# Optimization experiments

Measured on AMD Instinct MI355X. Metric: run time of the kernel, lower is better.

Reference implementation:

```python
import jax, jax.numpy as jnp
import numpy as np

EPS = 1e-6

def elu_feature_map(x):
    # phi(x) = elu(x) + 1 (always positive)
    return jax.nn.elu(x) + 1.0

def setup_inputs() -> dict:
    key = jax.random.key(0)
    kq, kk, kv = jax.random.split(key, 3)
    B, T, H, E = 2, 4096, 8, 64
    return {
        "query": jax.random.normal(kq, (B, T, H, E), dtype=jnp.float32),
        "key": jax.random.normal(kk, (B, T, H, E), dtype=jnp.float32),
        "value": jax.random.normal(kv, (B, T, H, E), dtype=jnp.float32),
    }

def reference(query, key, value):
    # b t h e -> b h t e
    q = jnp.transpose(query, (0, 2, 1, 3))
    k = jnp.transpose(key, (0, 2, 1, 3))
    v = jnp.transpose(value, (0, 2, 1, 3))
    Q = elu_feature_map(q)  # [b,h,t,e]
    K = elu_feature_map(k)  # [b,h,t,e]
    # Causal linear attention: running sums over the sequence axis.
    # KV_cum[t] = sum_{s<=t} K_s (outer) V_s  -> [b,h,t,e,d]
    kv = jnp.einsum('bhte,bhtd->bhted', K, v)
    kv_cum = jnp.cumsum(kv, axis=2)
    k_cum = jnp.cumsum(K, axis=2)  # [b,h,t,e]
    # Normalizer Z_t = 1 / (Q_t . sum_{s<=t} K_s + eps)
    Z = 1.0 / (jnp.einsum('bhte,bhte->bht', Q, k_cum) + EPS)
    out = jnp.einsum('bhte,bhted->bhtd', Q, kv_cum) * Z[..., None]
    # b h t d -> b t h d
    return jnp.transpose(out, (0, 2, 1, 3))
```

## Files before the change

### kernel.cpp

```cpp
#include <hip/hip_runtime.h>
#include <math.h>

#define B 2
#define T 4096
#define H 8
#define E 64
#define D 64
#define C 128
#define NC (T / C)
#define BH (B * H)
#define EPS 1e-6f
#define PT 132
#define PQ 72
#define PBT 200
typedef short short8 __attribute__((ext_vector_type(8)));
typedef short short4v __attribute__((ext_vector_type(4)));
typedef float f32x4 __attribute__((ext_vector_type(4)));

__device__ __forceinline__ float phi(float x) {
    return x > 0.0f ? x + 1.0f : __expf(x);
}
__device__ __forceinline__ ushort f2bf(float f) {
    uint u = __float_as_uint(f);
    return (ushort)((u + 0x7FFFu + ((u >> 16) & 1u)) >> 16);
}
__device__ __forceinline__ float bf2f(ushort h) {
    return __uint_as_float(((uint)h) << 16);
}

__global__ __launch_bounds__(256) void k_chunk_sums(
        const float* __restrict__ Kg, const float* __restrict__ Vg,
        float* __restrict__ SpartT, float* __restrict__ zpart,
        ushort* __restrict__ VTg) {
    int blk = blockIdx.x;
    int bh = blk / NC, c = blk % NC;
    int b = bh / H, h = bh % H;
    int t0 = c * C;
    __shared__ ushort sKt[E][PT];
    __shared__ ushort sVt[D][PT];
    int tid = threadIdx.x;
    int lane = tid & 63, w = tid >> 6;
    const float4* Kg4 = (const float4*)Kg;
    const float4* Vg4 = (const float4*)Vg;

    for (int l = tid; l < C * E / 4; l += 256) {
        int i = l >> 4, e4 = l & 15;
        size_t g = ((size_t)(b * T + t0 + i) * H + h) * 16 + e4;
        float4 kv = Kg4[g];
        float pk[4] = {phi(kv.x), phi(kv.y), phi(kv.z), phi(kv.w)};
        float4 vv = Vg4[g];
        float pv[4] = {vv.x, vv.y, vv.z, vv.w};
        #pragma unroll
        for (int cc = 0; cc < 4; ++cc) {
            sKt[e4 * 4 + cc][i] = f2bf(pk[cc]);
            sVt[e4 * 4 + cc][i] = f2bf(pv[cc]);
        }
    }
    __syncthreads();

    float* Sp = SpartT + (size_t)blk * (E * D);
    #pragma unroll
    for (int tt = 0; tt < 4; ++tt) {
        int idx = w * 4 + tt;
        int mt = idx >> 2, nt = idx & 3;
        int am = mt * 16 + (lane & 15);
        int bn = nt * 16 + (lane & 15);
        int kb = (lane >> 4) * 8;
        f32x4 acc = {};
        #pragma unroll
        for (int ks = 0; ks < 4; ++ks) {
            short8 a  = *(const short8*)&sVt[am][ks * 32 + kb];
            short8 bb = *(const short8*)&sKt[bn][ks * 32 + kb];
            acc = __builtin_amdgcn_mfma_f32_16x16x32_bf16(a, bb, acc, 0, 0, 0);
        }
        #pragma unroll
        for (int r = 0; r < 4; ++r) {
            int drow = mt * 16 + (lane >> 4) * 4 + r;
            Sp[drow * E + bn] = acc[r];
        }
    }
    ushort* vt = VTg + (size_t)blk * (C * D);
    for (int l = tid; l < C * D / 8; l += 256) {
        int d = l >> 4, p = l & 15;
        *(short8*)&vt[d * C + p * 8] = *(const short8*)&sVt[d][p * 8];
    }
    if (tid < E) {
        float s = 0.0f;
        #pragma unroll
        for (int p = 0; p < 16; ++p) {
            short8 v = *(const short8*)&sKt[tid][p * 8];
            #pragma unroll
            for (int j = 0; j < 8; ++j) s += bf2f((ushort)v[j]);
        }
        zpart[(size_t)blk * E + tid] = s;
    }
}

__global__ __launch_bounds__(256) void k_scan(
        float* __restrict__ SpartT, float* __restrict__ zpart) {
    int bh  = blockIdx.x / 17;
    int sub = blockIdx.x % 17;
    int tid = threadIdx.x;
    if (sub < 16) {
        int l = sub * 256 + tid;
        float* base = SpartT + (size_t)bh * NC * (E * D) + l;
        float vals[NC];
        #pragma unroll
        for (int c = 0; c < NC; ++c) vals[c] = base[(size_t)c * (E * D)];
        float run = 0.0f;
        #pragma unroll
        for (int c = 0; c < NC; ++c) {
            base[(size_t)c * (E * D)] = run;
            run += vals[c];
        }
    } else if (tid < E) {
        float* base = zpart + (size_t)bh * NC * E + tid;
        float vals[NC];
        #pragma unroll
        for (int c = 0; c < NC; ++c) vals[c] = base[(size_t)c * E];
        float run = 0.0f;
        #pragma unroll
        for (int c = 0; c < NC; ++c) {
            base[(size_t)c * E] = run;
            run += vals[c];
        }
    }
}

__global__ __launch_bounds__(512, 4) void k_output(
        const float* __restrict__ Qg, const float* __restrict__ Kg,
        const ushort* __restrict__ VTg, const float* __restrict__ SpartT,
        const float* __restrict__ zpart, float* __restrict__ Og) {
    int blk = blockIdx.x;
    int bh = blk / NC, c = blk % NC;
    int b = bh / H, h = bh % H;
    int t0 = c * C;

    __shared__ ushort sQ[C][PQ];
    __shared__ ushort sKB[64 * PBT];
    __shared__ ushort sA[C][C];
    __shared__ float  sDen[C];
    __shared__ float  sZ[E];

    int tid = threadIdx.x;
    int lane = tid & 63;
    int w = tid >> 6;

    const float4* Qg4 = (const float4*)Qg;
    const float4* Kg4 = (const float4*)Kg;

    for (int l = tid; l < C * 8; l += 512) {
        int i = l >> 3, e8 = l & 7;
        size_t g = ((size_t)(b * T + t0 + i) * H + h) * 16 + e8 * 2;
        float4 qa = Qg4[g], qb = Qg4[g + 1];
        short8 qv;
        qv[0] = (short)f2bf(phi(qa.x)); qv[1] = (short)f2bf(phi(qa.y));
        qv[2] = (short)f2bf(phi(qa.z)); qv[3] = (short)f2bf(phi(qa.w));
        qv[4] = (short)f2bf(phi(qb.x)); qv[5] = (short)f2bf(phi(qb.y));
        qv[6] = (short)f2bf(phi(qb.z)); qv[7] = (short)f2bf(phi(qb.w));
        *(short8*)&sQ[i][e8 * 8] = qv;
        float4 ka = Kg4[g], kb = Kg4[g + 1];
        short8 kv;
        kv[0] = (short)f2bf(phi(ka.x)); kv[1] = (short)f2bf(phi(ka.y));
        kv[2] = (short)f2bf(phi(ka.z)); kv[3] = (short)f2bf(phi(ka.w));
        kv[4] = (short)f2bf(phi(kb.x)); kv[5] = (short)f2bf(phi(kb.y));
        kv[6] = (short)f2bf(phi(kb.z)); kv[7] = (short)f2bf(phi(kb.w));
        *(short8*)&sKB[i * PQ + e8 * 8] = kv;
    }
    {
        short8 zz = {0, 0, 0, 0, 0, 0, 0, 0};
        ushort* af = (ushort*)sA;
        #pragma unroll
        for (int it = 0; it < 4; ++it)
            *(short8*)&af[(tid + 512 * it) * 8] = zz;
    }
    const short8* vt8 = (const short8*)(VTg + (size_t)blk * (C * D));
    short8 vtreg[2];
    #pragma unroll
    for (int it = 0; it < 2; ++it) vtreg[it] = vt8[tid * 2 + it];
    const float4* Sp4 = (const float4*)(SpartT + (size_t)blk * (E * D));
    float4 s0reg[2];
    #pragma unroll
    for (int it = 0; it < 2; ++it) s0reg[it] = Sp4[tid * 2 + it];
    if (tid < E) sZ[tid] = zpart[(size_t)blk * E + tid];
    __syncthreads();

    for (int idx = w; idx < 36; idx += 8) {
        int tr = 0;
        while ((tr + 1) * (tr + 2) / 2 <= idx) ++tr;
        int tc = idx - tr * (tr + 1) / 2;
        int am = tr * 16 + (lane & 15);
        int bn = tc * 16 + (lane & 15);
        int kb = (lane >> 4) * 8;
        f32x4 acc = {};
        #pragma unroll
        for (int ks = 0; ks < 2; ++ks) {
            short8 a  = *(const short8*)&sQ[am][ks * 32 + kb];
            short8 bb = *(const short8*)&sKB[bn * PQ + ks * 32 + kb];
            acc = __builtin_amdgcn_mfma_f32_16x16x32_bf16(a, bb, acc, 0, 0, 0);
        }
        int colb = tc * 16 + (lane & 15);
        #pragma unroll
        for (int r = 0; r < 4; ++r) {
            int row = tr * 16 + (lane >> 4) * 4 + r;
            if (tr == tc && colb > row) continue;
            sA[row][colb ^ ((row & 7) << 3)] = f2bf(acc[r]);
        }
    }
    __syncthreads();

    #pragma unroll
    for (int it = 0; it < 2; ++it) {
        int idx = tid * 2 + it;
        int d = idx >> 4, p = idx & 15;
        *(short8*)&sKB[d * PBT + p * 8] = vtreg[it];
    }
    #pragma unroll
    for (int it = 0; it < 2; ++it) {
        int idx = tid * 2 + it;
        int d = idx >> 4, e0 = (idx & 15) * 4;
        float4 s = s0reg[it];
        short4v sv;
        sv[0] = (short)f2bf(s.x); sv[1] = (short)f2bf(s.y);
        sv[2] = (short)f2bf(s.z); sv[3] = (short)f2bf(s.w);
        *(short4v*)&sKB[d * PBT + 128 + e0] = sv;
    }
    if (tid < 256) {
        int row = tid >> 1, hf = tid & 1;
        float s = 0.0f;
        const ushort* ar = &sA[row][hf * 64];
        #pragma unroll
        for (int q8 = 0; q8 < 8; ++q8) {
            int cq = (q8 + row) & 7;
            short8 v = *(const short8*)&ar[cq * 8];
            #pragma unroll
            for (int j = 0; j < 8; ++j) s += bf2f((ushort)v[j]);
        }
        const ushort* qr = &sQ[row][0];
        #pragma unroll
        for (int e = 0; e < 32; ++e) {
            int ee = hf * 32 + e;
            s += bf2f(qr[ee]) * sZ[ee];
        }
        s += __shfl_xor(s, 1);
        if (hf == 0) sDen[row] = s;
    }
    __syncthreads();

    {
        int tcn = w & 3;
        int trb = w >> 2;
        int ncol = tcn * 16 + (lane & 15);
        int g8 = (lane >> 4) * 8;
        #pragma unroll
        for (int rt = 0; rt < 4; ++rt) {
            int tr = trb + rt * 2;
            int m0 = tr * 16;
            int arow = m0 + (lane & 15);
            int aswz = arow & 7;
            f32x4 acc = {};
            int smax = (m0 + 15) >> 5;
            for (int s = 0; s <= smax; ++s) {
                int chunk = s * 4 + (lane >> 4);
                short8 a  = *(const short8*)&sA[arow][(chunk ^ aswz) * 8];
                short8 bb = *(const short8*)&sKB[ncol * PBT + s * 32 + g8];
                acc = __builtin_amdgcn_mfma_f32_16x16x32_bf16(a, bb, acc, 0, 0, 0);
            }
            #pragma unroll
            for (int s = 0; s < 2; ++s) {
                short8 a  = *(const short8*)&sQ[arow][s * 32 + g8];
                short8 bb = *(const short8*)&sKB[ncol * PBT + 128 + s * 32 + g8];
                acc = __builtin_amdgcn_mfma_f32_16x16x32_bf16(a, bb, acc, 0, 0, 0);
            }
            #pragma unroll
            for (int r = 0; r < 4; ++r) {
                int row = m0 + (lane >> 4) * 4 + r;
                float z = 1.0f / (sDen[row] + EPS);
                Og[((size_t)(b * T + t0 + row) * H + h) * 64 + ncol] = acc[r] * z;
            }
        }
    }
}

extern "C" void kernel_launch(void* const* d_in, const int* in_sizes, int n_in,
                              void* d_out, int out_size, void* d_ws, size_t ws_size,
                              hipStream_t stream) {
    const float* q = (const float*)d_in[0];
    const float* k = (const float*)d_in[1];
    const float* v = (const float*)d_in[2];
    float* out = (float*)d_out;

    float*  SpartT = (float*)d_ws;
    float*  zpart  = SpartT + (size_t)BH * NC * E * D;
    ushort* VTg    = (ushort*)(zpart + (size_t)BH * NC * E);

    k_chunk_sums<<<BH * NC, 256, 0, stream>>>(k, v, SpartT, zpart, VTg);
    k_scan<<<BH * 17, 256, 0, stream>>>(SpartT, zpart);
    k_output<<<BH * NC, 512, 0, stream>>>(q, k, VTg, SpartT, zpart, out);
}
```

Baseline: 35.22 us.

## Fold normalizer into MFMA, cache phi(K) in bf16, restructure output tiling

```diff
diff --git a/kernel.cpp b/kernel.cpp
--- a/kernel.cpp
+++ b/kernel.cpp
@@ -1,4 +1,5 @@
 #include <hip/hip_runtime.h>
+#include <hip/hip_bf16.h>
 #include <math.h>
 
 #define B 2
@@ -13,25 +14,26 @@
 #define PT 132
 #define PQ 72
 #define PBT 200
+
 typedef short short8 __attribute__((ext_vector_type(8)));
-typedef short short4v __attribute__((ext_vector_type(4)));
 typedef float f32x4 __attribute__((ext_vector_type(4)));
 
 __device__ __forceinline__ float phi(float x) {
     return x > 0.0f ? x + 1.0f : __expf(x);
+}
+__device__ __forceinline__ uint pk2(float a, float b) {
+    __hip_bfloat162 h = __float22bfloat162_rn(make_float2(a, b));
+    union { __hip_bfloat162 h2; uint u; } cv; cv.h2 = h; return cv.u;
 }
 __device__ __forceinline__ ushort f2bf(float f) {
     uint u = __float_as_uint(f);
     return (ushort)((u + 0x7FFFu + ((u >> 16) & 1u)) >> 16);
 }
-__device__ __forceinline__ float bf2f(ushort h) {
-    return __uint_as_float(((uint)h) << 16);
-}
 
 __global__ __launch_bounds__(256) void k_chunk_sums(
         const float* __restrict__ Kg, const float* __restrict__ Vg,
         float* __restrict__ SpartT, float* __restrict__ zpart,
-        ushort* __restrict__ VTg) {
+        ushort* __restrict__ VTg, ushort* __restrict__ PKg) {
     int blk = blockIdx.x;
     int bh = blk / NC, c = blk % NC;
     int b = bh / H, h = bh % H;
@@ -42,75 +44,81 @@
     int lane = tid & 63, w = tid >> 6;
     const float4* Kg4 = (const float4*)Kg;
     const float4* Vg4 = (const float4*)Vg;
-
-    for (int l = tid; l < C * E / 4; l += 256) {
-        int i = l >> 4, e4 = l & 15;
-        size_t g = ((size_t)(b * T + t0 + i) * H + h) * 16 + e4;
-        float4 kv = Kg4[g];
-        float pk[4] = {phi(kv.x), phi(kv.y), phi(kv.z), phi(kv.w)};
-        float4 vv = Vg4[g];
-        float pv[4] = {vv.x, vv.y, vv.z, vv.w};
+    uint2* PK2 = (uint2*)(PKg + (size_t)blk * (C * E));
+
+    for (int l = tid; l < (C / 2) * 16; l += 256) {
+        int i2 = l >> 4, e4 = l & 15;
+        int t = i2 * 2;
+        size_t g0 = ((size_t)(b * T + t0 + t) * H + h) * 16 + e4;
+        size_t g1 = g0 + H * 16;
+        float4 ka = Kg4[g0], kb = Kg4[g1];
+        float4 va = Vg4[g0], vb = Vg4[g1];
+        float pk0[4] = {phi(ka.x), phi(ka.y), phi(ka.z), phi(ka.w)};
+        float pk1[4] = {phi(kb.x), phi(kb.y), phi(kb.z), phi(kb.w)};
+        float pv0[4] = {va.x, va.y, va.z, va.w};
+        float pv1[4] = {vb.x, vb.y, vb.z, vb.w};
         #pragma unroll
         for (int cc = 0; cc < 4; ++cc) {
-            sKt[e4 * 4 + cc][i] = f2bf(pk[cc]);
-            sVt[e4 * 4 + cc][i] = f2bf(pv[cc]);
-        }
-    }
-    __syncthreads();
-
-    float* Sp = SpartT + (size_t)blk * (E * D);
-    #pragma unroll
-    for (int tt = 0; tt < 4; ++tt) {
-        int idx = w * 4 + tt;
-        int mt = idx >> 2, nt = idx & 3;
-        int am = mt * 16 + (lane & 15);
-        int bn = nt * 16 + (lane & 15);
-        int kb = (lane >> 4) * 8;
-        f32x4 acc = {};
-        #pragma unroll
+            *(uint*)&sKt[e4 * 4 + cc][t] = pk2(pk0[cc], pk1[cc]);
+            *(uint*)&sVt[e4 * 4 + cc][t] = pk2(pv0[cc], pv1[cc]);
+        }
+        PK2[t * 16 + e4]       = make_uint2(pk2(pk0[0], pk0[1]), pk2(pk0[2], pk0[3]));
+        PK2[(t + 1) * 16 + e4] = make_uint2(pk2(pk1[0], pk1[1]), pk2(pk1[2], pk1[3]));
+    }
+    __syncthreads();
+
+    {
+        int g = lane >> 4, cl = lane & 15;
+        int mt = w;
+        f32x4 acc[4] = {};
         for (int ks = 0; ks < 4; ++ks) {
-            short8 a  = *(const short8*)&sVt[am][ks * 32 + kb];
-            short8 bb = *(const short8*)&sKt[bn][ks * 32 + kb];
-            acc = __builtin_amdgcn_mfma_f32_16x16x32_bf16(a, bb, acc, 0, 0, 0);
-        }
-        #pragma unroll
-        for (int r = 0; r < 4; ++r) {
-            int drow = mt * 16 + (lane >> 4) * 4 + r;
-            Sp[drow * E + bn] = acc[r];
+            short8 a = *(const short8*)&sKt[mt * 16 + cl][ks * 32 + g * 8];
+            #pragma unroll
+            for (int nt = 0; nt < 4; ++nt) {
+                short8 bb = *(const short8*)&sVt[nt * 16 + cl][ks * 32 + g * 8];
+                acc[nt] = __builtin_amdgcn_mfma_f32_16x16x32_bf16(a, bb, acc[nt], 0, 0, 0);
+            }
+        }
+        float* Sp = SpartT + (size_t)blk * (E * D);
+        #pragma unroll
+        for (int nt = 0; nt < 4; ++nt) {
+            int d = nt * 16 + cl;
+            *(float4*)&Sp[d * E + mt * 16 + g * 4] =
+                make_float4(acc[nt][0], acc[nt][1], acc[nt][2], acc[nt][3]);
         }
     }
     ushort* vt = VTg + (size_t)blk * (C * D);
-    for (int l = tid; l < C * D / 8; l += 256) {
-        int d = l >> 4, p = l & 15;
-        *(short8*)&vt[d * C + p * 8] = *(const short8*)&sVt[d][p * 8];
-    }
+    for (int l = tid; l < C * D / 8; l += 256)
+        *(short8*)&vt[(l >> 4) * C + (l & 15) * 8] = *(const short8*)&sVt[l >> 4][(l & 15) * 8];
     if (tid < E) {
         float s = 0.0f;
         #pragma unroll
         for (int p = 0; p < 16; ++p) {
             short8 v = *(const short8*)&sKt[tid][p * 8];
             #pragma unroll
-            for (int j = 0; j < 8; ++j) s += bf2f((ushort)v[j]);
+            for (int j = 0; j < 8; ++j) s += __uint_as_float(((uint)(ushort)v[j]) << 16);
         }
         zpart[(size_t)blk * E + tid] = s;
     }
 }
 
 __global__ __launch_bounds__(256) void k_scan(
-        float* __restrict__ SpartT, float* __restrict__ zpart) {
+        const float* __restrict__ SpartT, float* __restrict__ zpart,
+        ushort* __restrict__ S0bf) {
     int bh  = blockIdx.x / 17;
     int sub = blockIdx.x % 17;
     int tid = threadIdx.x;
     if (sub < 16) {
         int l = sub * 256 + tid;
-        float* base = SpartT + (size_t)bh * NC * (E * D) + l;
+        const float* base = SpartT + (size_t)bh * NC * (E * D) + l;
+        ushort* obase = S0bf + (size_t)bh * NC * (E * D) + l;
         float vals[NC];
         #pragma unroll
         for (int c = 0; c < NC; ++c) vals[c] = base[(size_t)c * (E * D)];
         float run = 0.0f;
         #pragma unroll
         for (int c = 0; c < NC; ++c) {
-            base[(size_t)c * (E * D)] = run;
+            obase[(size_t)c * (E * D)] = f2bf(run);
             run += vals[c];
         }
     } else if (tid < E) {
@@ -128,8 +136,8 @@
 }
 
 __global__ __launch_bounds__(512, 4) void k_output(
-        const float* __restrict__ Qg, const float* __restrict__ Kg,
-        const ushort* __restrict__ VTg, const float* __restrict__ SpartT,
+        const float* __restrict__ Qg, const ushort* __restrict__ PKg,
+        const ushort* __restrict__ VTg, const ushort* __restrict__ S0bf,
         const float* __restrict__ zpart, float* __restrict__ Og) {
     int blk = blockIdx.x;
     int bh = blk / NC, c = blk % NC;
@@ -137,147 +145,109 @@
     int t0 = c * C;
 
     __shared__ ushort sQ[C][PQ];
-    __shared__ ushort sKB[64 * PBT];
+    __shared__ ushort sKB[13000];
     __shared__ ushort sA[C][C];
-    __shared__ float  sDen[C];
-    __shared__ float  sZ[E];
 
     int tid = threadIdx.x;
     int lane = tid & 63;
     int w = tid >> 6;
+    int g = lane >> 4, cl = lane & 15;
 
     const float4* Qg4 = (const float4*)Qg;
-    const float4* Kg4 = (const float4*)Kg;
 
     for (int l = tid; l < C * 8; l += 512) {
         int i = l >> 3, e8 = l & 7;
-        size_t g = ((size_t)(b * T + t0 + i) * H + h) * 16 + e8 * 2;
-        float4 qa = Qg4[g], qb = Qg4[g + 1];
-        short8 qv;
-        qv[0] = (short)f2bf(phi(qa.x)); qv[1] = (short)f2bf(phi(qa.y));
-        qv[2] = (short)f2bf(phi(qa.z)); qv[3] = (short)f2bf(phi(qa.w));
-        qv[4] = (short)f2bf(phi(qb.x)); qv[5] = (short)f2bf(phi(qb.y));
-        qv[6] = (short)f2bf(phi(qb.z)); qv[7] = (short)f2bf(phi(qb.w));
-        *(short8*)&sQ[i][e8 * 8] = qv;
-        float4 ka = Kg4[g], kb = Kg4[g + 1];
-        short8 kv;
-        kv[0] = (short)f2bf(phi(ka.x)); kv[1] = (short)f2bf(phi(ka.y));
-        kv[2] = (short)f2bf(phi(ka.z)); kv[3] = (short)f2bf(phi(ka.w));
-        kv[4] = (short)f2bf(phi(kb.x)); kv[5] = (short)f2bf(phi(kb.y));
-        kv[6] = (short)f2bf(phi(kb.z)); kv[7] = (short)f2bf(phi(kb.w));
-        *(short8*)&sKB[i * PQ + e8 * 8] = kv;
-    }
-    {
-        short8 zz = {0, 0, 0, 0, 0, 0, 0, 0};
+        size_t gg = ((size_t)(b * T + t0 + i) * H + h) * 16 + e8 * 2;
+        float4 qa = Qg4[gg], qb = Qg4[gg + 1];
+        uint4 qv = make_uint4(pk2(phi(qa.x), phi(qa.y)), pk2(phi(qa.z), phi(qa.w)),
+                              pk2(phi(qb.x), phi(qb.y)), pk2(phi(qb.z), phi(qb.w)));
+        *(uint4*)&sQ[i][e8 * 8] = qv;
+    }
+    const short8* pk8 = (const short8*)(PKg + (size_t)blk * (C * E));
+    for (int l = tid; l < C * 8; l += 512)
+        *(short8*)&sKB[(l >> 3) * PQ + (l & 7) * 8] = pk8[l];
+    {
+        uint4 zz = make_uint4(0, 0, 0, 0);
         ushort* af = (ushort*)sA;
         #pragma unroll
         for (int it = 0; it < 4; ++it)
-            *(short8*)&af[(tid + 512 * it) * 8] = zz;
+            *(uint4*)&af[(tid + 512 * it) * 8] = zz;
     }
     const short8* vt8 = (const short8*)(VTg + (size_t)blk * (C * D));
-    short8 vtreg[2];
-    #pragma unroll
-    for (int it = 0; it < 2; ++it) vtreg[it] = vt8[tid * 2 + it];
-    const float4* Sp4 = (const float4*)(SpartT + (size_t)blk * (E * D));
-    float4 s0reg[2];
-    #pragma unroll
-    for (int it = 0; it < 2; ++it) s0reg[it] = Sp4[tid * 2 + it];
-    if (tid < E) sZ[tid] = zpart[(size_t)blk * E + tid];
+    short8 vt0 = vt8[tid * 2], vt1 = vt8[tid * 2 + 1];
+    short8 s0reg = ((const short8*)(S0bf + (size_t)blk * (E * D)))[tid];
+    float zreg = (tid < E) ? zpart[(size_t)blk * E + tid] : 0.0f;
     __syncthreads();
 
     for (int idx = w; idx < 36; idx += 8) {
         int tr = 0;
         while ((tr + 1) * (tr + 2) / 2 <= idx) ++tr;
         int tc = idx - tr * (tr + 1) / 2;
-        int am = tr * 16 + (lane & 15);
-        int bn = tc * 16 + (lane & 15);
-        int kb = (lane >> 4) * 8;
         f32x4 acc = {};
         #pragma unroll
         for (int ks = 0; ks < 2; ++ks) {
-            short8 a  = *(const short8*)&sQ[am][ks * 32 + kb];
-            short8 bb = *(const short8*)&sKB[bn * PQ + ks * 32 + kb];
-            acc = __builtin_amdgcn_mfma_f32_16x16x32_bf16(a, bb, acc, 0, 0, 0);
-        }
-        int colb = tc * 16 + (lane & 15);
+            short8 a  = *(const short8*)&sKB[(tc * 16 + cl) * PQ + ks * 32 + g * 8];
+            short8 bq = *(const short8*)&sQ[tr * 16 + cl][ks * 32 + g * 8];
+            acc = __builtin_amdgcn_mfma_f32_16x16x32_bf16(a, bq, acc, 0, 0, 0);
+        }
+        int iq = tr * 16 + cl;
+        int j0 = tc * 16 + g * 4;
+        float v0 = (j0 + 0 <= iq) ? acc[0] : 0.0f;
+        float v1 = (j0 + 1 <= iq) ? acc[1] : 0.0f;
+        float v2 = (j0 + 2 <= iq) ? acc[2] : 0.0f;
+        float v3 = (j0 + 3 <= iq) ? acc[3] : 0.0f;
+        int pb = (tc * 2 + (g >> 1)) ^ (iq & 7);
+        *(uint2*)&sA[iq][pb * 8 + (g & 1) * 4] = make_uint2(pk2(v0, v1), pk2(v2, v3));
+    }
+    __syncthreads();
+
+    {
+        int i0 = tid * 2, i1 = tid * 2 + 1;
+        *(short8*)&sKB[(i0 >> 4) * PBT + (i0 & 15) * 8] = vt0;
+        *(short8*)&sKB[(i1 >> 4) * PBT + (i1 & 15) * 8] = vt1;
+        *(short8*)&sKB[(tid >> 3) * PBT + 128 + (tid & 7) * 8] = s0reg;
+        if (tid < E) sKB[64 * PBT + 128 + tid] = f2bf(zreg);
+        else if (tid < E + 16) {
+            short8 ones = {16256, 16256, 16256, 16256, 16256, 16256, 16256, 16256};
+            *(short8*)&sKB[64 * PBT + (tid - E) * 8] = ones;
+        }
+    }
+    __syncthreads();
+
+    {
+        const int permv[8] = {0, 1, 2, 3, 6, 7, 4, 5};
+        int mt = permv[w];
+        int m0 = mt * 16;
+        int arow = m0 + cl;
+        int aswz = arow & 7;
+        int smax = (m0 + 15) >> 5;
+        f32x4 acc[5] = {};
+        for (int s = 0; s <= smax; ++s) {
+            short8 a = *(const short8*)&sA[arow][(((s * 4 + g) ^ aswz)) * 8];
+            #pragma unroll
+            for (int nt = 0; nt < 5; ++nt) {
+                short8 bb = *(const short8*)&sKB[(nt * 16 + cl) * PBT + s * 32 + g * 8];
+                acc[nt] = __builtin_amdgcn_mfma_f32_16x16x32_bf16(a, bb, acc[nt], 0, 0, 0);
+            }
+        }
+        #pragma unroll
+        for (int s2 = 0; s2 < 2; ++s2) {
+            short8 a = *(const short8*)&sQ[arow][s2 * 32 + g * 8];
+            #pragma unroll
+            for (int nt = 0; nt < 5; ++nt) {
+                short8 bb = *(const short8*)&sKB[(nt * 16 + cl) * PBT + 128 + s2 * 32 + g * 8];
+                acc[nt] = __builtin_amdgcn_mfma_f32_16x16x32_bf16(a, bb, acc[nt], 0, 0, 0);
+            }
+        }
         #pragma unroll
         for (int r = 0; r < 4; ++r) {
-            int row = tr * 16 + (lane >> 4) * 4 + r;
-            if (tr == tc && colb > row) continue;
-            sA[row][colb ^ ((row & 7) << 3)] = f2bf(acc[r]);
-        }
-    }
-    __syncthreads();
-
-    #pragma unroll
-    for (int it = 0; it < 2; ++it) {
-        int idx = tid * 2 + it;
-        int d = idx >> 4, p = idx & 15;
-        *(short8*)&sKB[d * PBT + p * 8] = vtreg[it];
-    }
-    #pragma unroll
-    for (int it = 0; it < 2; ++it) {
-        int idx = tid * 2 + it;
-        int d = idx >> 4, e0 = (idx & 15) * 4;
-        float4 s = s0reg[it];
-        short4v sv;
-        sv[0] = (short)f2bf(s.x); sv[1] = (short)f2bf(s.y);
-        sv[2] = (short)f2bf(s.z); sv[3] = (short)f2bf(s.w);
-        *(short4v*)&sKB[d * PBT + 128 + e0] = sv;
-    }
-    if (tid < 256) {
-        int row = tid >> 1, hf = tid & 1;
-        float s = 0.0f;
-        const ushort* ar = &sA[row][hf * 64];
-        #pragma unroll
-        for (int q8 = 0; q8 < 8; ++q8) {
-            int cq = (q8 + row) & 7;
-            short8 v = *(const short8*)&ar[cq * 8];
-            #pragma unroll
-            for (int j = 0; j < 8; ++j) s += bf2f((ushort)v[j]);
-        }
-        const ushort* qr = &sQ[row][0];
-        #pragma unroll
-        for (int e = 0; e < 32; ++e) {
-            int ee = hf * 32 + e;
-            s += bf2f(qr[ee]) * sZ[ee];
-        }
-        s += __shfl_xor(s, 1);
-        if (hf == 0) sDen[row] = s;
-    }
-    __syncthreads();
-
-    {
-        int tcn = w & 3;
-        int trb = w >> 2;
-        int ncol = tcn * 16 + (lane & 15);
-        int g8 = (lane >> 4) * 8;
-        #pragma unroll
-        for (int rt = 0; rt < 4; ++rt) {
-            int tr = trb + rt * 2;
-            int m0 = tr * 16;
-            int arow = m0 + (lane & 15);
-            int aswz = arow & 7;
-            f32x4 acc = {};
-            int smax = (m0 + 15) >> 5;
-            for (int s = 0; s <= smax; ++s) {
-                int chunk = s * 4 + (lane >> 4);
-                short8 a  = *(const short8*)&sA[arow][(chunk ^ aswz) * 8];
-                short8 bb = *(const short8*)&sKB[ncol * PBT + s * 32 + g8];
-                acc = __builtin_amdgcn_mfma_f32_16x16x32_bf16(a, bb, acc, 0, 0, 0);
-            }
-            #pragma unroll
-            for (int s = 0; s < 2; ++s) {
-                short8 a  = *(const short8*)&sQ[arow][s * 32 + g8];
-                short8 bb = *(const short8*)&sKB[ncol * PBT + 128 + s * 32 + g8];
-                acc = __builtin_amdgcn_mfma_f32_16x16x32_bf16(a, bb, acc, 0, 0, 0);
-            }
-            #pragma unroll
-            for (int r = 0; r < 4; ++r) {
-                int row = m0 + (lane >> 4) * 4 + r;
-                float z = 1.0f / (sDen[row] + EPS);
-                Og[((size_t)(b * T + t0 + row) * H + h) * 64 + ncol] = acc[r] * z;
-            }
+            float den = __shfl(acc[4][r], lane & 48);
+            float zi = 1.0f / (den + EPS);
+            int row = m0 + g * 4 + r;
+            size_t ga = ((size_t)(b * T + t0 + row) * H + h) * 64;
+            #pragma unroll
+            for (int nt = 0; nt < 4; ++nt)
+                Og[ga + nt * 16 + cl] = acc[nt][r] * zi;
         }
     }
 }
@@ -293,8 +263,10 @@
     float*  SpartT = (float*)d_ws;
     float*  zpart  = SpartT + (size_t)BH * NC * E * D;
     ushort* VTg    = (ushort*)(zpart + (size_t)BH * NC * E);
-
-    k_chunk_sums<<<BH * NC, 256, 0, stream>>>(k, v, SpartT, zpart, VTg);
-    k_scan<<<BH * 17, 256, 0, stream>>>(SpartT, zpart);
-    k_output<<<BH * NC, 512, 0, stream>>>(q, k, VTg, SpartT, zpart, out);
-}
+    ushort* PKg    = VTg + (size_t)BH * NC * C * D;
+    ushort* S0bf   = PKg + (size_t)BH * NC * C * E;
+
+    k_chunk_sums<<<BH * NC, 256, 0, stream>>>(k, v, SpartT, zpart, VTg, PKg);
+    k_scan<<<BH * 17, 256, 0, stream>>>(SpartT, zpart, S0bf);
+    k_output<<<BH * NC, 512, 0, stream>>>(q, PKg, VTg, S0bf, zpart, out);
+}
```

Result: faster. 32.76 us (-7.0%).
